# Kernel optimization log

Measured on AMD Instinct MI355X. Metric: run time of the kernel, lower is better.

## Reference

```python
import jax, jax.numpy as jnp
import numpy as np

# Module config (init_kwargs), window_type='1d' (forward default)
GROUPS = 4
WIN = (1, 9)      # search_window_1d (ps_y, ps_x)
DIL = (1, 1)      # search_dilate_1d
S = WIN[0] * WIN[1]  # search_pixels = 9

B, C, H, W = 2, 256, 80, 160


def setup_inputs() -> dict:
    key = jax.random.key(0)
    k1, k2, k3, k4 = jax.random.split(key, 4)
    return {
        "left_feature": jax.random.normal(k1, (B, C, H, W), jnp.float32),
        "right_feature": jax.random.normal(k2, (B, C, H, W), jnp.float32),
        "flow": jax.random.normal(k3, (B, 2, H, W), jnp.float32) * 2.0,
        "extra_offset": jax.random.normal(k4, (B, 2 * S, H, W), jnp.float32),
    }


def _window_offsets():
    # torch.meshgrid(arange(-rx,rx+1,dx), arange(-ry,ry+1,dy), indexing='xy')
    ry, rx = (WIN[0] // 2) * DIL[0], (WIN[1] // 2) * DIL[1]
    xg, yg = np.meshgrid(np.arange(-rx, rx + 1, DIL[1]),
                         np.arange(-ry, ry + 1, DIL[0]), indexing="xy")
    off = np.stack([xg, yg], 0).reshape(2, -1).T  # (S, 2) as (x, y)
    return jnp.asarray(off, jnp.float32)


def _bilinear_sample(img, coords):
    """F.grid_sample(mode='bilinear', padding_mode='zeros', align_corners=True)
    with absolute pixel coords (torchvision raft's grid_sample normalizes by
    2*x/(W-1)-1, which is exactly identity sampling at absolute coords).
    img: (B,C,H,W); coords: (B,S,H,W,2) absolute (x,y). Returns (B,C,S,H,W)."""
    Bv, Cv, Hv, Wv = img.shape
    x, y = coords[..., 0], coords[..., 1]
    x0f = jnp.floor(x); y0f = jnp.floor(y)
    wx = (x - x0f)[:, None]  # (B,1,S,H,W)
    wy = (y - y0f)[:, None]
    x0 = x0f.astype(jnp.int32); y0 = y0f.astype(jnp.int32)
    imgf = img.reshape(Bv, Cv, Hv * Wv)

    def gather(yi, xi):
        valid = (xi >= 0) & (xi < Wv) & (yi >= 0) & (yi < Hv)
        idx = jnp.clip(yi, 0, Hv - 1) * Wv + jnp.clip(xi, 0, Wv - 1)
        v = jax.vmap(lambda im, ix: im[:, ix])(imgf, idx)  # (B,C,S,H,W)
        return v * valid[:, None].astype(img.dtype)

    v00 = gather(y0, x0)
    v01 = gather(y0, x0 + 1)
    v10 = gather(y0 + 1, x0)
    v11 = gather(y0 + 1, x0 + 1)
    return (v00 * (1 - wx) * (1 - wy) + v01 * wx * (1 - wy)
            + v10 * (1 - wx) * wy + v11 * wx * wy)


def reference(left_feature, right_feature, flow, extra_offset):
    Bv, Cv, Hv, Wv = left_feature.shape
    gC = Cv // GROUPS
    # make_coords_grid: channel order (x, y), absolute pixel coords
    yy, xx = jnp.meshgrid(jnp.arange(Hv, dtype=jnp.float32),
                          jnp.arange(Wv, dtype=jnp.float32), indexing="ij")
    base = jnp.stack([xx, yy], -1)[None, None] \
        + jnp.transpose(flow, (0, 2, 3, 1))[:, None]            # (B,1,H,W,2)
    extra = jnp.transpose(extra_offset.reshape(Bv, S, 2, Hv, Wv),
                          (0, 1, 3, 4, 2))                        # (B,S,H,W,2)
    coords = base + _window_offsets()[None, :, None, None, :] + extra
    # All groups share identical window/dilation, so sample all channels once.
    sampled = _bilinear_sample(right_feature, coords)  # (B,C,S,H,W)
    leftg = left_feature.reshape(Bv, GROUPS, gC, Hv, Wv)
    sampg = sampled.reshape(Bv, GROUPS, gC, S, Hv, Wv)
    # mean over group channels of left * sampled
    corr = jnp.einsum("bgchw,bgcshw->bgshw", leftg, sampg) / gC
    return corr.reshape(Bv, GROUPS * S, Hv, Wv)
```

## Files before the change

kernel.cpp:

```cpp
#include <hip/hip_runtime.h>

#define Bc   2
#define Cc   256
#define Hc   80
#define Wc   160
#define Gc   4
#define Sc   9
#define GCc  64
#define HWc  (Hc * Wc)
#define H2c  (Hc / 2)
#define WTc  (Wc / 32)
#define NW   4
#define CPW  16

#define PROWS   20
#define TSTRIDE 66
#define TDW     (PROWS * TSTRIDE)

typedef float f4 __attribute__((ext_vector_type(4)));
typedef _Float16 h2 __attribute__((ext_vector_type(2)));
typedef unsigned u2 __attribute__((ext_vector_type(2)));

static __device__ __forceinline__ unsigned pk(float a, float b) {
    return __builtin_bit_cast(unsigned, __builtin_amdgcn_cvt_pkrtz(a, b));
}
static __device__ __forceinline__ float dot2(unsigned w, unsigned v, float c) {
#if __has_builtin(__builtin_amdgcn_fdot2)
    return __builtin_amdgcn_fdot2(__builtin_bit_cast(h2, w),
                                  __builtin_bit_cast(h2, v), c, false);
#else
    h2 hw = __builtin_bit_cast(h2, w), hv = __builtin_bit_cast(h2, v);
    return c + (float)hw[0] * (float)hv[0] + (float)hw[1] * (float)hv[1];
#endif
}

#define CFENCE() asm volatile("" ::: "memory")

__global__ __launch_bounds__(256, 3)
void aoc_corr_kernel(const float* __restrict__ left,
                     const float* __restrict__ right,
                     const float* __restrict__ flow,
                     const float* __restrict__ extra,
                     float* __restrict__ out)
{
    __shared__ unsigned tile[NW][2][TDW];

    int bid = blockIdx.x;
    int wt = bid % WTc; bid /= WTc;
    int h2i = bid % H2c; bid /= H2c;
    int g  = bid % Gc;  bid /= Gc;
    int b  = bid;

    const int tid  = threadIdx.x;
    const int wid  = tid >> 6;
    const int lane = tid & 63;
    const int r    = lane >> 5;
    const int col  = lane & 31;
    const int h    = h2i * 2 + r;
    const int w    = wt * 32 + col;
    const int pix  = h * Wc + w;

    const float* flowb = flow + (size_t)b * 2 * HWc;
    const float bx = (float)w + flowb[pix];
    const float by = (float)h + flowb[HWc + pix];

    int   xb9[Sc], y09[Sc], y19[Sc];
    float w00[Sc], w01[Sc], w10[Sc], w11[Sc];
    int minX = 1 << 30, maxX = -(1 << 30), minY = 1 << 30, maxY = -(1 << 30);

    const float* exb = extra + (size_t)b * (2 * Sc) * HWc + pix;
#pragma unroll
    for (int s = 0; s < Sc; ++s) {
        const float ex = exb[(size_t)(2 * s) * HWc];
        const float ey = exb[(size_t)(2 * s + 1) * HWc];
        const float x = bx + (float)(s - 4) + ex;
        const float y = by + ey;

        const float x0f = floorf(x);
        const float y0f = floorf(y);
        const float fx = x - x0f;
        const float fy = y - y0f;
        const int x0 = (int)x0f;
        const int y0 = (int)y0f;
        const int y1 = y0 + 1;

        const int xb = min(max(x0, 0), Wc - 2);
        const float cA = (x0 == xb) ? (1.0f - fx) : ((x0 == -1)     ? fx          : 0.0f);
        const float cB = (x0 == xb) ? fx          : ((x0 == Wc - 1) ? (1.0f - fx) : 0.0f);
        const float r0 = (y0 >= 0 && y0 < Hc) ? (1.0f - fy) : 0.0f;
        const float r1 = (y1 >= 0 && y1 < Hc) ? fy          : 0.0f;
        const int yc0 = min(max(y0, 0), Hc - 1);
        const int yc1 = min(max(y1, 0), Hc - 1);

        w00[s] = cA * r0;  w01[s] = cB * r0;
        w10[s] = cA * r1;  w11[s] = cB * r1;
        xb9[s] = xb;  y09[s] = yc0;  y19[s] = yc1;

        minX = min(minX, xb);
        maxX = max(maxX, xb);
        minY = min(minY, min(yc0, yc1));
        maxY = max(maxY, max(yc0, yc1));
    }

#pragma unroll
    for (int k = 1; k < 64; k <<= 1) {
        minX = min(minX, __shfl_xor(minX, k));
        maxX = max(maxX, __shfl_xor(maxX, k));
        minY = min(minY, __shfl_xor(minY, k));
        maxY = max(maxY, __shfl_xor(maxY, k));
    }
    const int minX2 = min(minX, Wc - 64) & ~3;
    const bool valid = (maxY - minY + 1 <= PROWS) && (maxX - minX2 <= 62);

    const float* Rb = right + ((size_t)b * Cc + (size_t)(g * GCc + wid * CPW)) * HWc;
    const float* Lb = left  + ((size_t)b * Cc + (size_t)(g * GCc + wid * CPW)) * HWc + pix;

    float acc[Sc];
#pragma unroll
    for (int s = 0; s < Sc; ++s) acc[s] = 0.0f;

    if (valid) {
        unsigned wA[Sc], wB[Sc];
        int idx[Sc];
#pragma unroll
        for (int s = 0; s < Sc; ++s) {
            const int t  = y09[s] - minY;
            const int sB = y19[s] - y09[s];
            const float A0 = w00[s] + (sB ? 0.0f : w10[s]);
            const float A1 = sB ? w10[s] : 0.0f;
            const float B0 = w01[s] + (sB ? 0.0f : w11[s]);
            const float B1 = sB ? w11[s] : 0.0f;
            wA[s] = pk(A0, A1);
            wB[s] = pk(B0, B1);
            idx[s] = t * TSTRIDE + (xb9[s] - minX2);
        }

        const int ls  = lane >> 4;
        const int seg = lane & 15;
        int rowEl[6];
#pragma unroll
        for (int k = 0; k < 6; ++k)
            rowEl[k] = min(minY + 5 * ls + k, Hc - 1) * Wc + minX2 + seg * 4;

        f4 rv[6];
#pragma unroll
        for (int k = 0; k < 6; ++k) rv[k] = *(const f4*)(Rb + rowEl[k]);
        float lv = Lb[0];

#pragma unroll 1
        for (int c = 0; c < CPW; ++c) {
            unsigned* tw = tile[wid][c & 1];
            CFENCE();
#pragma unroll
            for (int j = 0; j < 5; ++j) {
                unsigned* q = tw + (5 * ls + j) * TSTRIDE + seg * 4;
                u2 lo = { pk(rv[j][0], rv[j + 1][0]), pk(rv[j][1], rv[j + 1][1]) };
                u2 hi = { pk(rv[j][2], rv[j + 1][2]), pk(rv[j][3], rv[j + 1][3]) };
                *(u2*)q       = lo;
                *(u2*)(q + 2) = hi;
            }
            CFENCE();
            float lvn = 0.0f;
            if (c + 1 < CPW) {
                const float* Rn = Rb + (size_t)(c + 1) * HWc;
#pragma unroll
                for (int k = 0; k < 6; ++k) rv[k] = *(const f4*)(Rn + rowEl[k]);
                lvn = Lb[(size_t)(c + 1) * HWc];
            }
#pragma unroll
            for (int s = 0; s < Sc; ++s) {
                const unsigned d0 = tw[idx[s]];
                const unsigned d1 = tw[idx[s] + 1];
                float sd = dot2(wA[s], d0, 0.0f);
                sd = dot2(wB[s], d1, sd);
                acc[s] = fmaf(lv, sd, acc[s]);
            }
            lv = lvn;
        }
    } else {
        int offA[Sc], offB[Sc];
#pragma unroll
        for (int s = 0; s < Sc; ++s) {
            offA[s] = y09[s] * Wc + xb9[s];
            offB[s] = y19[s] * Wc + xb9[s];
        }
        for (int c = 0; c < CPW; ++c) {
            const float lv = Lb[(size_t)c * HWc];
            const float* Rc = Rb + (size_t)c * HWc;
#pragma unroll
            for (int s = 0; s < Sc; ++s) {
                const float vA0 = Rc[offA[s]];
                const float vA1 = Rc[offA[s] + 1];
                const float vB0 = Rc[offB[s]];
                const float vB1 = Rc[offB[s] + 1];
                acc[s] += lv * (w00[s] * vA0 + w01[s] * vA1 +
                                w10[s] * vB0 + w11[s] * vB1);
            }
        }
    }

    float* red = (float*)&tile[0][0][0];
    __syncthreads();
    if (wid != 0) {
#pragma unroll
        for (int s = 0; s < Sc; ++s)
            red[((wid - 1) * Sc + s) * 64 + lane] = acc[s];
    }
    __syncthreads();
    if (wid == 0) {
        const float inv = 1.0f / (float)GCc;
        float* ob = out + ((size_t)b * Gc + g) * Sc * HWc + pix;
#pragma unroll
        for (int s = 0; s < Sc; ++s) {
            float v = acc[s];
#pragma unroll
            for (int ww = 1; ww < NW; ++ww)
                v += red[((ww - 1) * Sc + s) * 64 + lane];
            ob[(size_t)s * HWc] = v * inv;
        }
    }
}

extern "C" void kernel_launch(void* const* d_in, const int* in_sizes, int n_in,
                              void* d_out, int out_size, void* d_ws, size_t ws_size,
                              hipStream_t stream) {
    const float* left  = (const float*)d_in[0];
    const float* right = (const float*)d_in[1];
    const float* flow  = (const float*)d_in[2];
    const float* extra = (const float*)d_in[3];
    float* out = (float*)d_out;

    const int nblocks = Bc * Gc * H2c * WTc;
    aoc_corr_kernel<<<nblocks, NW * 64, 0, stream>>>(left, right, flow, extra, out);
}
```

Measured before the change: 57.06 us.

## Halve waves per block and software-pipeline LDS tile reads with inline ds_read2

Cuts the block from four waves to two, each now handling 32 channels instead of 16. The channel loop is restructured into a two-stage software pipeline: the tile for channel c+1 is written while channel c's LDS reads are in flight, and global loads run two channels ahead. LDS reads use inline ds_read2_b32 with precomputed LDS addresses, a manual lgkmcnt wait and sched_barrier, to cut address math and overlap LDS latency with global loads. Fewer waves per block means more serial work per wave and a smaller cross-wave reduction. The hand-coded waitcnt is fragile if the compiler reorders or emits more LDS operations.

```diff
diff --git a/kernel.cpp b/kernel.cpp
--- a/kernel.cpp
+++ b/kernel.cpp
@@ -10,8 +10,8 @@
 #define HWc  (Hc * Wc)
 #define H2c  (Hc / 2)
 #define WTc  (Wc / 32)
-#define NW   4
-#define CPW  16
+#define NW   2
+#define CPW  32
 
 #define PROWS   20
 #define TSTRIDE 66
@@ -20,6 +20,8 @@
 typedef float f4 __attribute__((ext_vector_type(4)));
 typedef _Float16 h2 __attribute__((ext_vector_type(2)));
 typedef unsigned u2 __attribute__((ext_vector_type(2)));
+typedef unsigned uv2 __attribute__((ext_vector_type(2)));
+typedef __attribute__((address_space(3))) unsigned* lup;
 
 static __device__ __forceinline__ unsigned pk(float a, float b) {
     return __builtin_bit_cast(unsigned, __builtin_amdgcn_cvt_pkrtz(a, b));
@@ -36,7 +38,45 @@
 
 #define CFENCE() asm volatile("" ::: "memory")
 
-__global__ __launch_bounds__(256, 3)
+#define PIPE_ITER(cI, VA)                                                   \
+  do {                                                                      \
+    uv2 pr[Sc];                                                             \
+    _Pragma("unroll")                                                       \
+    for (int s = 0; s < Sc; ++s)                                            \
+      asm volatile("ds_read2_b32 %0, %1 offset0:0 offset1:1"                \
+                   : "=v"(pr[s]) : "v"(VA[s]));                             \
+    CFENCE();                                                               \
+    {                                                                       \
+      unsigned* twn = twBase + (((cI) + 1) & 1) * TDW;                      \
+      _Pragma("unroll")                                                     \
+      for (int j = 0; j < 5; ++j) {                                         \
+        unsigned* q = twn + (5 * ls + j) * TSTRIDE + seg * 4;               \
+        u2 lo = { pk(rv[j][0], rv[j + 1][0]), pk(rv[j][1], rv[j + 1][1]) }; \
+        u2 hi = { pk(rv[j][2], rv[j + 1][2]), pk(rv[j][3], rv[j + 1][3]) }; \
+        *(u2*)q       = lo;                                                 \
+        *(u2*)(q + 2) = hi;                                                 \
+      }                                                                     \
+    }                                                                       \
+    CFENCE();                                                               \
+    float lvN = 0.0f;                                                       \
+    if ((cI) + 2 < CPW) {                                                   \
+      const float* Rn = Rb + (size_t)((cI) + 2) * HWc;                      \
+      _Pragma("unroll")                                                     \
+      for (int k = 0; k < 6; ++k) rv[k] = *(const f4*)(Rn + rowEl[k]);      \
+      lvN = Lb[(size_t)((cI) + 2) * HWc];                                   \
+    }                                                                       \
+    asm volatile("s_waitcnt lgkmcnt(10)" ::: "memory");                     \
+    __builtin_amdgcn_sched_barrier(0);                                      \
+    _Pragma("unroll")                                                       \
+    for (int s = 0; s < Sc; ++s) {                                          \
+      float sd = dot2(wA[s], pr[s].x, 0.0f);                                \
+      sd = dot2(wB[s], pr[s].y, sd);                                        \
+      acc[s] = fmaf(lvA, sd, acc[s]);                                       \
+    }                                                                       \
+    lvA = lvB; lvB = lvN;                                                   \
+  } while (0)
+
+__global__ __launch_bounds__(128, 4)
 void aoc_corr_kernel(const float* __restrict__ left,
                      const float* __restrict__ right,
                      const float* __restrict__ flow,
@@ -121,7 +161,7 @@
 
     if (valid) {
         unsigned wA[Sc], wB[Sc];
-        int idx[Sc];
+        unsigned va0[Sc], va1[Sc];
 #pragma unroll
         for (int s = 0; s < Sc; ++s) {
             const int t  = y09[s] - minY;
@@ -132,7 +172,9 @@
             const float B1 = sB ? w11[s] : 0.0f;
             wA[s] = pk(A0, A1);
             wB[s] = pk(B0, B1);
-            idx[s] = t * TSTRIDE + (xb9[s] - minX2);
+            const int idx = t * TSTRIDE + (xb9[s] - minX2);
+            va0[s] = (unsigned)(size_t)(lup)&tile[wid][0][idx];
+            va1[s] = va0[s] + TDW * 4;
         }
 
         const int ls  = lane >> 4;
@@ -142,40 +184,44 @@
         for (int k = 0; k < 6; ++k)
             rowEl[k] = min(minY + 5 * ls + k, Hc - 1) * Wc + minX2 + seg * 4;
 
+        unsigned* twBase = &tile[wid][0][0];
+
         f4 rv[6];
 #pragma unroll
         for (int k = 0; k < 6; ++k) rv[k] = *(const f4*)(Rb + rowEl[k]);
-        float lv = Lb[0];
+        float lvA = Lb[0];
+#pragma unroll
+        for (int j = 0; j < 5; ++j) {
+            unsigned* q = twBase + (5 * ls + j) * TSTRIDE + seg * 4;
+            u2 lo = { pk(rv[j][0], rv[j + 1][0]), pk(rv[j][1], rv[j + 1][1]) };
+            u2 hi = { pk(rv[j][2], rv[j + 1][2]), pk(rv[j][3], rv[j + 1][3]) };
+            *(u2*)q       = lo;
+            *(u2*)(q + 2) = hi;
+        }
+        CFENCE();
+#pragma unroll
+        for (int k = 0; k < 6; ++k) rv[k] = *(const f4*)(Rb + HWc + rowEl[k]);
+        float lvB = Lb[HWc];
 
 #pragma unroll 1
-        for (int c = 0; c < CPW; ++c) {
-            unsigned* tw = tile[wid][c & 1];
-            CFENCE();
-#pragma unroll
-            for (int j = 0; j < 5; ++j) {
-                unsigned* q = tw + (5 * ls + j) * TSTRIDE + seg * 4;
-                u2 lo = { pk(rv[j][0], rv[j + 1][0]), pk(rv[j][1], rv[j + 1][1]) };
-                u2 hi = { pk(rv[j][2], rv[j + 1][2]), pk(rv[j][3], rv[j + 1][3]) };
-                *(u2*)q       = lo;
-                *(u2*)(q + 2) = hi;
+        for (int cc = 0; cc < CPW - 1; cc += 2) {
+            PIPE_ITER(cc, va0);
+            if (cc + 1 < CPW - 1) PIPE_ITER(cc + 1, va1);
+        }
+        {
+            uv2 pr[Sc];
+#pragma unroll
+            for (int s = 0; s < Sc; ++s)
+                asm volatile("ds_read2_b32 %0, %1 offset0:0 offset1:1"
+                             : "=v"(pr[s]) : "v"(va1[s]));
+            asm volatile("s_waitcnt lgkmcnt(0)" ::: "memory");
+            __builtin_amdgcn_sched_barrier(0);
+#pragma unroll
+            for (int s = 0; s < Sc; ++s) {
+                float sd = dot2(wA[s], pr[s].x, 0.0f);
+                sd = dot2(wB[s], pr[s].y, sd);
+                acc[s] = fmaf(lvA, sd, acc[s]);
             }
-            CFENCE();
-            float lvn = 0.0f;
-            if (c + 1 < CPW) {
-                const float* Rn = Rb + (size_t)(c + 1) * HWc;
-#pragma unroll
-                for (int k = 0; k < 6; ++k) rv[k] = *(const f4*)(Rn + rowEl[k]);
-                lvn = Lb[(size_t)(c + 1) * HWc];
-            }
-#pragma unroll
-            for (int s = 0; s < Sc; ++s) {
-                const unsigned d0 = tw[idx[s]];
-                const unsigned d1 = tw[idx[s] + 1];
-                float sd = dot2(wA[s], d0, 0.0f);
-                sd = dot2(wB[s], d1, sd);
-                acc[s] = fmaf(lv, sd, acc[s]);
-            }
-            lv = lvn;
         }
     } else {
         int offA[Sc], offB[Sc];
```

Result: slower. 89.18 us (+56.3%).

## Deepen global-load prefetch to two channels ahead with even/odd register sets

Applied to the files above, without the earlier changes.

Replaces the single-buffered register prefetch (one channel ahead) with two register sets, so global loads for channel c+2 are in flight while channel c is packed into LDS and consumed. The loop is manually unrolled by two with fixed LDS buffers per parity, and an explicit lgkmcnt wait is added before each LDS store. This is meant to hide more global-memory latency per wave. In exchange it doubles the prefetch registers (12 f4 instead of 6), which may pressure the 3-blocks-per-SM launch bound and cause spills or lower occupancy.

```diff
diff --git a/kernel.cpp b/kernel.cpp
--- a/kernel.cpp
+++ b/kernel.cpp
@@ -36,6 +36,37 @@
 
 #define CFENCE() asm volatile("" ::: "memory")
 
+#define ITER2(cI, RV, LV, BUF)                                              \
+  do {                                                                      \
+    asm volatile("s_waitcnt lgkmcnt(0)" ::: "memory");                      \
+    _Pragma("unroll")                                                       \
+    for (int j = 0; j < 5; ++j) {                                           \
+      unsigned* q = twBase + (BUF) * TDW + (5 * ls + j) * TSTRIDE + seg * 4;\
+      u2 lo = { pk(RV[j][0], RV[j + 1][0]), pk(RV[j][1], RV[j + 1][1]) };   \
+      u2 hi = { pk(RV[j][2], RV[j + 1][2]), pk(RV[j][3], RV[j + 1][3]) };   \
+      *(u2*)q       = lo;                                                   \
+      *(u2*)(q + 2) = hi;                                                   \
+    }                                                                       \
+    CFENCE();                                                               \
+    if ((cI) + 2 < CPW) {                                                   \
+      const float* Rn = Rb + (size_t)((cI) + 2) * HWc;                      \
+      _Pragma("unroll")                                                     \
+      for (int k = 0; k < 6; ++k) RV[k] = *(const f4*)(Rn + rowEl[k]);      \
+    }                                                                       \
+    {                                                                       \
+      const unsigned* twr = twBase + (BUF) * TDW;                           \
+      _Pragma("unroll")                                                     \
+      for (int s = 0; s < Sc; ++s) {                                        \
+        const unsigned d0 = twr[idx[s]];                                    \
+        const unsigned d1 = twr[idx[s] + 1];                                \
+        float sd = dot2(wA[s], d0, 0.0f);                                   \
+        sd = dot2(wB[s], d1, sd);                                           \
+        acc[s] = fmaf(LV, sd, acc[s]);                                      \
+      }                                                                     \
+    }                                                                       \
+    if ((cI) + 2 < CPW) LV = Lb[(size_t)((cI) + 2) * HWc];                  \
+  } while (0)
+
 __global__ __launch_bounds__(256, 3)
 void aoc_corr_kernel(const float* __restrict__ left,
                      const float* __restrict__ right,
@@ -142,40 +173,20 @@
         for (int k = 0; k < 6; ++k)
             rowEl[k] = min(minY + 5 * ls + k, Hc - 1) * Wc + minX2 + seg * 4;
 
-        f4 rv[6];
-#pragma unroll
-        for (int k = 0; k < 6; ++k) rv[k] = *(const f4*)(Rb + rowEl[k]);
-        float lv = Lb[0];
+        unsigned* twBase = &tile[wid][0][0];
+
+        f4 rvE[6], rvO[6];
+#pragma unroll
+        for (int k = 0; k < 6; ++k) rvE[k] = *(const f4*)(Rb + rowEl[k]);
+#pragma unroll
+        for (int k = 0; k < 6; ++k) rvO[k] = *(const f4*)(Rb + HWc + rowEl[k]);
+        float lvE = Lb[0];
+        float lvO = Lb[HWc];
 
 #pragma unroll 1
-        for (int c = 0; c < CPW; ++c) {
-            unsigned* tw = tile[wid][c & 1];
-            CFENCE();
-#pragma unroll
-            for (int j = 0; j < 5; ++j) {
-                unsigned* q = tw + (5 * ls + j) * TSTRIDE + seg * 4;
-                u2 lo = { pk(rv[j][0], rv[j + 1][0]), pk(rv[j][1], rv[j + 1][1]) };
-                u2 hi = { pk(rv[j][2], rv[j + 1][2]), pk(rv[j][3], rv[j + 1][3]) };
-                *(u2*)q       = lo;
-                *(u2*)(q + 2) = hi;
-            }
-            CFENCE();
-            float lvn = 0.0f;
-            if (c + 1 < CPW) {
-                const float* Rn = Rb + (size_t)(c + 1) * HWc;
-#pragma unroll
-                for (int k = 0; k < 6; ++k) rv[k] = *(const f4*)(Rn + rowEl[k]);
-                lvn = Lb[(size_t)(c + 1) * HWc];
-            }
-#pragma unroll
-            for (int s = 0; s < Sc; ++s) {
-                const unsigned d0 = tw[idx[s]];
-                const unsigned d1 = tw[idx[s] + 1];
-                float sd = dot2(wA[s], d0, 0.0f);
-                sd = dot2(wB[s], d1, sd);
-                acc[s] = fmaf(lv, sd, acc[s]);
-            }
-            lv = lvn;
+        for (int cc = 0; cc < CPW; cc += 2) {
+            ITER2(cc,     rvE, lvE, 0);
+            ITER2(cc + 1, rvO, lvO, 1);
         }
     } else {
         int offA[Sc], offB[Sc];
```

Measured after the change: 58.43 us. 1.02x slower.
